# Kernel tuning notes

Hardware: AMD Instinct MI355X
Metric: run time of the kernel (lower is better)

The kernel has to match this reference:

```python
import jax, jax.numpy as jnp
import numpy as np

B = 1024      # batch
E = 1024      # encoding_dim
OUT = 34      # 17 joints x 2 coords


def setup_inputs() -> dict:
    key = jax.random.key(0)
    ks = jax.random.split(key, 8)
    s = 0.02  # weight init scale
    return {
        "h": jax.random.normal(ks[0], (B, E), dtype=jnp.float32),
        "c": jax.random.normal(ks[1], (B, E), dtype=jnp.float32),
        "W_ih": jax.random.normal(ks[2], (4 * E, E), dtype=jnp.float32) * s,
        "W_hh": jax.random.normal(ks[3], (4 * E, E), dtype=jnp.float32) * s,
        "b_ih": jax.random.normal(ks[4], (4 * E,), dtype=jnp.float32) * s,
        "b_hh": jax.random.normal(ks[5], (4 * E,), dtype=jnp.float32) * s,
        "W_out": jax.random.normal(ks[6], (OUT, E), dtype=jnp.float32) * s,
        "b_out": jax.random.normal(ks[7], (OUT,), dtype=jnp.float32) * s,
        "future_preds": 10,
    }


def reference(h, c, W_ih, W_hh, b_ih, b_hh, W_out, b_out, future_preds):
    E_ = h.shape[1]
    start = jnp.zeros_like(h)  # zeros=True start token

    def step(carry, _):
        h_t, c_t, x = carry
        # LSTMCell: gates in PyTorch order i, f, g, o
        gates = x @ W_ih.T + b_ih + h_t @ W_hh.T + b_hh  # [B, 4E]
        i = jax.nn.sigmoid(gates[:, 0 * E_:1 * E_])
        f = jax.nn.sigmoid(gates[:, 1 * E_:2 * E_])
        g = jnp.tanh(gates[:, 2 * E_:3 * E_])
        o = jax.nn.sigmoid(gates[:, 3 * E_:4 * E_])
        c_new = f * c_t + i * g
        h_new = o * jnp.tanh(c_new)
        return (h_new, c_new, h_new), h_new

    _, hs = jax.lax.scan(step, (h, c, start), None, length=future_preds)
    # hs: [T, B, E] -> [B, T, E]
    preds = jnp.transpose(hs, (1, 0, 2))
    return preds @ W_out.T + b_out  # [B, T, 34]
```

## Files before the change

kernel.cpp:

```cpp
#include <hip/hip_runtime.h>
#include <cstdint>
#include <cstddef>

#define E_DIM   1024
#define B_DIM   1024
#define HPITCH  1040
#define T_STEPS 10
#define OUT_DIM 34
#define OUT_PAD 48
#define HSTR    24
#define WSLICE  65536
#define HT_ROWS 256
#define DYN_LDS (WSLICE * 2 + HT_ROWS * HSTR * 2)
#define HSLOT  ((size_t)B_DIM * HPITCH)

typedef __attribute__((ext_vector_type(4))) float  f32x4;
typedef __attribute__((ext_vector_type(8))) __bf16 bf16x8;

__device__ __forceinline__ unsigned short f2bf(float f) {
    unsigned int u = __float_as_uint(f);
    u = (u + 0x7FFFu + ((u >> 16) & 1u)) >> 16;
    return (unsigned short)u;
}
__device__ __forceinline__ float sigmoid_(float x) { return 1.0f / (1.0f + __expf(-x)); }
__device__ __forceinline__ float tanh_(float x)    { return 2.0f / (1.0f + __expf(-2.0f * x)) - 1.0f; }

__global__ void prep_weights_frag(const float* __restrict__ W_ih, const float* __restrict__ W_hh,
                                  unsigned short* __restrict__ WsumF, unsigned short* __restrict__ WhhF) {
    const int bn = blockIdx.x >> 3, qtr = (blockIdx.x >> 1) & 3, half = blockIdx.x & 1;
    const int nt = threadIdx.x >> 6, lane = threadIdx.x & 63;
    const int j = lane & 15, q = lane >> 4;
    const int srow = nt * E_DIM + bn * 16 + j;
    const float* wi = W_ih + (size_t)srow * E_DIM;
    const float* wh = W_hh + (size_t)srow * E_DIM;
    const size_t dstb = (size_t)bn * 65536 + (size_t)qtr * 16384 + nt * 512 + lane * 8;
#pragma unroll
    for (int ks8i = 0; ks8i < 4; ++ks8i) {
        const int ks8 = half * 4 + ks8i;
        const int k = qtr * 256 + ks8 * 32 + q * 8;
        float4 i0 = *(const float4*)(wi + k);
        float4 i1 = *(const float4*)(wi + k + 4);
        float4 h0 = *(const float4*)(wh + k);
        float4 h1 = *(const float4*)(wh + k + 4);
        unsigned short* ds = WsumF + dstb + ks8 * 2048;
        unsigned short* dh = WhhF  + dstb + ks8 * 2048;
        ds[0] = f2bf(i0.x + h0.x); ds[1] = f2bf(i0.y + h0.y);
        ds[2] = f2bf(i0.z + h0.z); ds[3] = f2bf(i0.w + h0.w);
        ds[4] = f2bf(i1.x + h1.x); ds[5] = f2bf(i1.y + h1.y);
        ds[6] = f2bf(i1.z + h1.z); ds[7] = f2bf(i1.w + h1.w);
        dh[0] = f2bf(h0.x); dh[1] = f2bf(h0.y); dh[2] = f2bf(h0.z); dh[3] = f2bf(h0.w);
        dh[4] = f2bf(h1.x); dh[5] = f2bf(h1.y); dh[6] = f2bf(h1.z); dh[7] = f2bf(h1.w);
    }
}

__global__ void prep_state(const float* __restrict__ h0, const float* __restrict__ c0,
                           const float* __restrict__ W_out,
                           const float* __restrict__ b_ih, const float* __restrict__ b_hh,
                           unsigned short* __restrict__ hbuf, unsigned short* __restrict__ Woutp,
                           float* __restrict__ bperm, float* __restrict__ C) {
    const int b = blockIdx.x;
    const int t = threadIdx.x;
    if (b < 1024) {
        const size_t src = ((size_t)b * 256 + t) * 4;
        float4 hv = *(const float4*)(h0 + src);
        const size_t i = (size_t)b * HPITCH + t * 4;
        hbuf[i + 0] = f2bf(hv.x);
        hbuf[i + 1] = f2bf(hv.y);
        hbuf[i + 2] = f2bf(hv.z);
        hbuf[i + 3] = f2bf(hv.w);
    } else if (b < 1072) {
        const int o = b - 1024;
        const int k = t * 4;
        float4 w = make_float4(0.f, 0.f, 0.f, 0.f);
        if (o < OUT_DIM) w = *(const float4*)(W_out + (size_t)o * E_DIM + k);
        const size_t dst = (size_t)o * E_DIM + k;
        Woutp[dst + 0] = f2bf(w.x);
        Woutp[dst + 1] = f2bf(w.y);
        Woutp[dst + 2] = f2bf(w.z);
        Woutp[dst + 3] = f2bf(w.w);
    } else if (b < 1088) {
        const int n = (b - 1072) * 256 + t;
        const int g = (n >> 4) & 3;
        const int e = ((n >> 6) << 4) | (n & 15);
        const int srow = g * E_DIM + e;
        bperm[n] = b_ih[srow] + b_hh[srow];
    } else {
        const int m = b - 1088;
        const int e0 = t * 4;
        float4 v = *(const float4*)(c0 + (size_t)m * E_DIM + e0);
        const int bm = m >> 7, wave = (m >> 5) & 3, mt = (m >> 4) & 1, q = (m >> 2) & 3, r = m & 3;
        const float vv[4] = {v.x, v.y, v.z, v.w};
#pragma unroll
        for (int ii = 0; ii < 4; ++ii) {
            const int e = e0 + ii;
            const int bn = e >> 4, jj = e & 15;
            const int lane = q * 16 + jj;
            C[(((size_t)(bn * 8 + bm) * 4 + wave) * 64 + lane) * 8 + mt * 4 + r] = vv[ii];
        }
    }
}

__global__ __launch_bounds__(512, 2) void lstm_step(
    const unsigned short* __restrict__ WF,
    const float* __restrict__ bp,
    const unsigned short* __restrict__ Hin,
    float* __restrict__ C,
    unsigned short* __restrict__ Hout)
{
    extern __shared__ __align__(16) unsigned short smem[];
    unsigned short* Wlds = smem;
    unsigned short* Ht   = smem + WSLICE;

    const int tid  = threadIdx.x;
    const int w    = tid >> 6;
    const int lane = tid & 63;
    const int bn = blockIdx.x;
    const int g  = blockIdx.y;
    const int j  = lane & 15;
    const int q  = lane >> 4;

    f32x4 acc[2][4];
#pragma unroll
    for (int a = 0; a < 2; ++a)
#pragma unroll
        for (int b = 0; b < 4; ++b) acc[a][b] = (f32x4){0.f, 0.f, 0.f, 0.f};

    const int nb = bn * 64 + j;
    const float bi = bp[nb +  0];
    const float bf = bp[nb + 16];
    const float bg = bp[nb + 32];
    const float bo = bp[nb + 48];
    const int obm = g * 2 + (w >> 2), owv = w & 3;
    const size_t cbase = (((size_t)(bn * 8 + obm) * 4 + owv) * 64 + lane) * 8;
    float4 cold0 = *(const float4*)(C + cbase);
    float4 cold1 = *(const float4*)(C + cbase + 4);

    const unsigned short* arow0 = Hin + (size_t)(g * 256 + w * 32 + j) * HPITCH + q * 8;
    const unsigned short* arow1 = arow0 + (size_t)16 * HPITCH;
    const unsigned short* wsrc  = WF + (size_t)bn * WSLICE;

    {
        uint4 wreg[8];
#pragma unroll
        for (int r2 = 0; r2 < 2; ++r2) {
#pragma unroll
            for (int i = 0; i < 8; ++i)
                wreg[i] = *(const uint4*)(wsrc + ((r2 * 8 + i) * 512 + tid) * 8);
#pragma unroll
            for (int i = 0; i < 8; ++i)
                *(uint4*)(Wlds + ((r2 * 8 + i) * 512 + tid) * 8) = wreg[i];
        }
    }

    uint4 ra[8][2];
#pragma unroll
    for (int p = 0; p < 8; ++p) {
        ra[p][0] = *(const uint4*)(arow0 + p * 32);
        ra[p][1] = *(const uint4*)(arow1 + p * 32);
    }
    __syncthreads();

    for (int qtr = 0; qtr < 4; ++qtr) {
        const unsigned short* wb = Wlds + qtr * 16384 + lane * 8;
#pragma unroll
        for (int ks8 = 0; ks8 < 8; ++ks8) {
            const int ks = qtr * 8 + ks8;
            bf16x8 av0 = __builtin_bit_cast(bf16x8, ra[ks8][0]);
            bf16x8 av1 = __builtin_bit_cast(bf16x8, ra[ks8][1]);
            bf16x8 bv[4];
#pragma unroll
            for (int nt = 0; nt < 4; ++nt)
                bv[nt] = *(const bf16x8*)(wb + (ks8 * 4 + nt) * 512);
#pragma unroll
            for (int nt = 0; nt < 4; ++nt) {
                acc[0][nt] = __builtin_amdgcn_mfma_f32_16x16x32_bf16(av0, bv[nt], acc[0][nt], 0, 0, 0);
                acc[1][nt] = __builtin_amdgcn_mfma_f32_16x16x32_bf16(av1, bv[nt], acc[1][nt], 0, 0, 0);
            }
            if (ks < 24) {
                ra[ks8][0] = *(const uint4*)(arow0 + (ks + 8) * 32);
                ra[ks8][1] = *(const uint4*)(arow1 + (ks + 8) * 32);
            }
        }
    }

    float4 cnew[2];
    const float coldv[2][4] = {{cold0.x, cold0.y, cold0.z, cold0.w},
                               {cold1.x, cold1.y, cold1.z, cold1.w}};
#pragma unroll
    for (int mt = 0; mt < 2; ++mt) {
#pragma unroll
        for (int r = 0; r < 4; ++r) {
            const float iv = sigmoid_(acc[mt][0][r] + bi);
            const float fv = sigmoid_(acc[mt][1][r] + bf);
            const float gv = tanh_(acc[mt][2][r] + bg);
            const float ov = sigmoid_(acc[mt][3][r] + bo);
            const float cn = fv * coldv[mt][r] + iv * gv;
            cnew[mt][r] = cn;
            const int rowl = w * 32 + mt * 16 + q * 4 + r;
            Ht[rowl * HSTR + j] = f2bf(ov * tanh_(cn));
        }
    }
    *(float4*)(C + cbase)     = cnew[0];
    *(float4*)(C + cbase + 4) = cnew[1];
    __syncthreads();

    {
        const int row = tid >> 1, part = tid & 1;
        uint4 v = *(const uint4*)(Ht + row * HSTR + part * 8);
        *(uint4*)(Hout + (size_t)(g * 256 + row) * HPITCH + bn * 16 + part * 8) = v;
    }
}

__global__ __launch_bounds__(256) void proj_kernel(
    const unsigned short* __restrict__ Hs,
    const unsigned short* __restrict__ Wo,
    const float* __restrict__ b_out,
    float* __restrict__ Out)
{
    __shared__ float red[4][32][OUT_PAD];

    const int tid = threadIdx.x, wave = tid >> 6, lane = tid & 63;
    const int j = lane & 15, q = lane >> 4;
    const int t  = blockIdx.y;
    const int bb = blockIdx.x;
    const unsigned short* Hbase = Hs + (size_t)t * HSLOT + (size_t)bb * 32 * HPITCH;
    const int k0 = wave * 256;

    f32x4 acc[2][3];
#pragma unroll
    for (int a = 0; a < 2; ++a)
#pragma unroll
        for (int b = 0; b < 3; ++b) acc[a][b] = (f32x4){0.f, 0.f, 0.f, 0.f};

#pragma unroll
    for (int kk = 0; kk < 256; kk += 32) {
        const int kc = k0 + kk + q * 8;
        bf16x8 av[2], bv[3];
#pragma unroll
        for (int mt = 0; mt < 2; ++mt)
            av[mt] = *(const bf16x8*)(Hbase + (size_t)(mt * 16 + j) * HPITCH + kc);
#pragma unroll
        for (int nt = 0; nt < 3; ++nt)
            bv[nt] = *(const bf16x8*)(Wo + (size_t)(nt * 16 + j) * E_DIM + kc);
#pragma unroll
        for (int mt = 0; mt < 2; ++mt)
#pragma unroll
            for (int nt = 0; nt < 3; ++nt)
                acc[mt][nt] = __builtin_amdgcn_mfma_f32_16x16x32_bf16(av[mt], bv[nt], acc[mt][nt], 0, 0, 0);
    }

#pragma unroll
    for (int mt = 0; mt < 2; ++mt)
#pragma unroll
        for (int nt = 0; nt < 3; ++nt)
#pragma unroll
            for (int r = 0; r < 4; ++r)
                red[wave][mt * 16 + q * 4 + r][nt * 16 + j] = acc[mt][nt][r];
    __syncthreads();

#pragma unroll
    for (int ii = 0; ii < 6; ++ii) {
        const int idx = tid * 6 + ii;
        const int row = idx / OUT_PAD, o = idx % OUT_PAD;
        if (o < OUT_DIM) {
            const float s = red[0][row][o] + red[1][row][o] + red[2][row][o] + red[3][row][o];
            Out[((size_t)(bb * 32 + row) * T_STEPS + t) * OUT_DIM + o] = s + b_out[o];
        }
    }
}

extern "C" void kernel_launch(void* const* d_in, const int* in_sizes, int n_in,
                              void* d_out, int out_size, void* d_ws, size_t ws_size,
                              hipStream_t stream) {
    (void)in_sizes; (void)n_in; (void)out_size; (void)ws_size;
    const float* h     = (const float*)d_in[0];
    const float* c     = (const float*)d_in[1];
    const float* W_ih  = (const float*)d_in[2];
    const float* W_hh  = (const float*)d_in[3];
    const float* b_ih  = (const float*)d_in[4];
    const float* b_hh  = (const float*)d_in[5];
    const float* W_out = (const float*)d_in[6];
    const float* b_out = (const float*)d_in[7];
    float* out = (float*)d_out;

    char* ws = (char*)d_ws;
    unsigned short* WsumF = (unsigned short*)(ws + 0);
    unsigned short* WhhF  = (unsigned short*)(ws + 8388608);
    float*          bperm = (float*)(ws + 16777216);
    unsigned short* Woutp = (unsigned short*)(ws + 16842752);
    float*          cbuf  = (float*)(ws + 16941056);
    unsigned short* hs    = (unsigned short*)(ws + 21135360);

    hipFuncSetAttribute((const void*)lstm_step,
                        hipFuncAttributeMaxDynamicSharedMemorySize, DYN_LDS);

    prep_weights_frag<<<512, 256, 0, stream>>>(W_ih, W_hh, WsumF, WhhF);
    prep_state<<<2112, 256, 0, stream>>>(h, c, W_out, b_ih, b_hh, hs, Woutp, bperm, cbuf);

    lstm_step<<<dim3(64, 4), 512, DYN_LDS, stream>>>(WhhF, bperm, hs, cbuf, hs + HSLOT);
    for (int t = 1; t < T_STEPS; ++t)
        lstm_step<<<dim3(64, 4), 512, DYN_LDS, stream>>>(WsumF, bperm,
                                                         hs + (size_t)t * HSLOT,
                                                         cbuf,
                                                         hs + (size_t)(t + 1) * HSLOT);

    proj_kernel<<<dim3(32, T_STEPS), 256, 0, stream>>>(hs + HSLOT, Woutp, b_out, out);
}
```

Measured before the change: 275.6 us.

## Overlap second-half weight load with MFMA compute and merge prep kernels

The step kernel now stages only the first half of its weight slice into LDS before computing. The second half is fetched into registers while the first half's MFMAs run, then written to LDS after a barrier, hiding part of the global load latency. The two prep kernels are also merged into one launch to save launch overhead. The trade-off is an extra barrier mid-loop and longer register live ranges across the first half of the compute.

New measurement: 367.5 us. +33.4%, slower.

```diff
diff --git a/kernel.cpp b/kernel.cpp
--- a/kernel.cpp
+++ b/kernel.cpp
@@ -10,6 +10,7 @@
 #define OUT_PAD 48
 #define HSTR    24
 #define WSLICE  65536
+#define WHALF   32768
 #define HT_ROWS 256
 #define DYN_LDS (WSLICE * 2 + HT_ROWS * HSTR * 2)
 #define HSLOT  ((size_t)B_DIM * HPITCH)
@@ -25,41 +26,43 @@
 __device__ __forceinline__ float sigmoid_(float x) { return 1.0f / (1.0f + __expf(-x)); }
 __device__ __forceinline__ float tanh_(float x)    { return 2.0f / (1.0f + __expf(-2.0f * x)) - 1.0f; }
 
-__global__ void prep_weights_frag(const float* __restrict__ W_ih, const float* __restrict__ W_hh,
-                                  unsigned short* __restrict__ WsumF, unsigned short* __restrict__ WhhF) {
-    const int bn = blockIdx.x >> 3, qtr = (blockIdx.x >> 1) & 3, half = blockIdx.x & 1;
-    const int nt = threadIdx.x >> 6, lane = threadIdx.x & 63;
-    const int j = lane & 15, q = lane >> 4;
-    const int srow = nt * E_DIM + bn * 16 + j;
-    const float* wi = W_ih + (size_t)srow * E_DIM;
-    const float* wh = W_hh + (size_t)srow * E_DIM;
-    const size_t dstb = (size_t)bn * 65536 + (size_t)qtr * 16384 + nt * 512 + lane * 8;
-#pragma unroll
-    for (int ks8i = 0; ks8i < 4; ++ks8i) {
-        const int ks8 = half * 4 + ks8i;
-        const int k = qtr * 256 + ks8 * 32 + q * 8;
-        float4 i0 = *(const float4*)(wi + k);
-        float4 i1 = *(const float4*)(wi + k + 4);
-        float4 h0 = *(const float4*)(wh + k);
-        float4 h1 = *(const float4*)(wh + k + 4);
-        unsigned short* ds = WsumF + dstb + ks8 * 2048;
-        unsigned short* dh = WhhF  + dstb + ks8 * 2048;
-        ds[0] = f2bf(i0.x + h0.x); ds[1] = f2bf(i0.y + h0.y);
-        ds[2] = f2bf(i0.z + h0.z); ds[3] = f2bf(i0.w + h0.w);
-        ds[4] = f2bf(i1.x + h1.x); ds[5] = f2bf(i1.y + h1.y);
-        ds[6] = f2bf(i1.z + h1.z); ds[7] = f2bf(i1.w + h1.w);
-        dh[0] = f2bf(h0.x); dh[1] = f2bf(h0.y); dh[2] = f2bf(h0.z); dh[3] = f2bf(h0.w);
-        dh[4] = f2bf(h1.x); dh[5] = f2bf(h1.y); dh[6] = f2bf(h1.z); dh[7] = f2bf(h1.w);
-    }
-}
-
-__global__ void prep_state(const float* __restrict__ h0, const float* __restrict__ c0,
-                           const float* __restrict__ W_out,
-                           const float* __restrict__ b_ih, const float* __restrict__ b_hh,
-                           unsigned short* __restrict__ hbuf, unsigned short* __restrict__ Woutp,
-                           float* __restrict__ bperm, float* __restrict__ C) {
-    const int b = blockIdx.x;
+__global__ void prep_all(const float* __restrict__ W_ih, const float* __restrict__ W_hh,
+                         const float* __restrict__ h0, const float* __restrict__ c0,
+                         const float* __restrict__ W_out,
+                         const float* __restrict__ b_ih, const float* __restrict__ b_hh,
+                         unsigned short* __restrict__ WsumF, unsigned short* __restrict__ WhhF,
+                         unsigned short* __restrict__ hbuf, unsigned short* __restrict__ Woutp,
+                         float* __restrict__ bperm, float* __restrict__ C) {
+    const int blk = blockIdx.x;
     const int t = threadIdx.x;
+    if (blk < 512) {
+        const int bn = blk >> 3, qtr = (blk >> 1) & 3, half = blk & 1;
+        const int nt = t >> 6, lane = t & 63;
+        const int j = lane & 15, q = lane >> 4;
+        const int srow = nt * E_DIM + bn * 16 + j;
+        const float* wi = W_ih + (size_t)srow * E_DIM;
+        const float* wh = W_hh + (size_t)srow * E_DIM;
+        const size_t dstb = (size_t)bn * 65536 + (size_t)qtr * 16384 + nt * 512 + lane * 8;
+#pragma unroll
+        for (int ks8i = 0; ks8i < 4; ++ks8i) {
+            const int ks8 = half * 4 + ks8i;
+            const int k = qtr * 256 + ks8 * 32 + q * 8;
+            float4 i0 = *(const float4*)(wi + k);
+            float4 i1 = *(const float4*)(wi + k + 4);
+            float4 h0v = *(const float4*)(wh + k);
+            float4 h1v = *(const float4*)(wh + k + 4);
+            unsigned short* ds = WsumF + dstb + ks8 * 2048;
+            unsigned short* dh = WhhF  + dstb + ks8 * 2048;
+            ds[0] = f2bf(i0.x + h0v.x); ds[1] = f2bf(i0.y + h0v.y);
+            ds[2] = f2bf(i0.z + h0v.z); ds[3] = f2bf(i0.w + h0v.w);
+            ds[4] = f2bf(i1.x + h1v.x); ds[5] = f2bf(i1.y + h1v.y);
+            ds[6] = f2bf(i1.z + h1v.z); ds[7] = f2bf(i1.w + h1v.w);
+            dh[0] = f2bf(h0v.x); dh[1] = f2bf(h0v.y); dh[2] = f2bf(h0v.z); dh[3] = f2bf(h0v.w);
+            dh[4] = f2bf(h1v.x); dh[5] = f2bf(h1v.y); dh[6] = f2bf(h1v.z); dh[7] = f2bf(h1v.w);
+        }
+        return;
+    }
+    const int b = blk - 512;
     if (b < 1024) {
         const size_t src = ((size_t)b * 256 + t) * 4;
         float4 hv = *(const float4*)(h0 + src);
@@ -139,18 +142,13 @@
     const unsigned short* arow1 = arow0 + (size_t)16 * HPITCH;
     const unsigned short* wsrc  = WF + (size_t)bn * WSLICE;
 
-    {
-        uint4 wreg[8];
-#pragma unroll
-        for (int r2 = 0; r2 < 2; ++r2) {
-#pragma unroll
-            for (int i = 0; i < 8; ++i)
-                wreg[i] = *(const uint4*)(wsrc + ((r2 * 8 + i) * 512 + tid) * 8);
-#pragma unroll
-            for (int i = 0; i < 8; ++i)
-                *(uint4*)(Wlds + ((r2 * 8 + i) * 512 + tid) * 8) = wreg[i];
-        }
-    }
+    uint4 wreg[8];
+#pragma unroll
+    for (int i = 0; i < 8; ++i)
+        wreg[i] = *(const uint4*)(wsrc + (i * 512 + tid) * 8);
+#pragma unroll
+    for (int i = 0; i < 8; ++i)
+        *(uint4*)(Wlds + (i * 512 + tid) * 8) = wreg[i];
 
     uint4 ra[8][2];
 #pragma unroll
@@ -160,26 +158,41 @@
     }
     __syncthreads();
 
-    for (int qtr = 0; qtr < 4; ++qtr) {
-        const unsigned short* wb = Wlds + qtr * 16384 + lane * 8;
-#pragma unroll
-        for (int ks8 = 0; ks8 < 8; ++ks8) {
-            const int ks = qtr * 8 + ks8;
-            bf16x8 av0 = __builtin_bit_cast(bf16x8, ra[ks8][0]);
-            bf16x8 av1 = __builtin_bit_cast(bf16x8, ra[ks8][1]);
-            bf16x8 bv[4];
-#pragma unroll
-            for (int nt = 0; nt < 4; ++nt)
-                bv[nt] = *(const bf16x8*)(wb + (ks8 * 4 + nt) * 512);
-#pragma unroll
-            for (int nt = 0; nt < 4; ++nt) {
-                acc[0][nt] = __builtin_amdgcn_mfma_f32_16x16x32_bf16(av0, bv[nt], acc[0][nt], 0, 0, 0);
-                acc[1][nt] = __builtin_amdgcn_mfma_f32_16x16x32_bf16(av1, bv[nt], acc[1][nt], 0, 0, 0);
+    for (int half = 0; half < 2; ++half) {
+        if (half == 0) {
+#pragma unroll
+            for (int i = 0; i < 8; ++i)
+                wreg[i] = *(const uint4*)(wsrc + WHALF + (i * 512 + tid) * 8);
+        }
+#pragma unroll
+        for (int qq = 0; qq < 2; ++qq) {
+            const int qtr = half * 2 + qq;
+            const unsigned short* wb = Wlds + qtr * 16384 + lane * 8;
+#pragma unroll
+            for (int ks8 = 0; ks8 < 8; ++ks8) {
+                const int ks = qtr * 8 + ks8;
+                bf16x8 av0 = __builtin_bit_cast(bf16x8, ra[ks8][0]);
+                bf16x8 av1 = __builtin_bit_cast(bf16x8, ra[ks8][1]);
+                bf16x8 bv[4];
+#pragma unroll
+                for (int nt = 0; nt < 4; ++nt)
+                    bv[nt] = *(const bf16x8*)(wb + (ks8 * 4 + nt) * 512);
+#pragma unroll
+                for (int nt = 0; nt < 4; ++nt) {
+                    acc[0][nt] = __builtin_amdgcn_mfma_f32_16x16x32_bf16(av0, bv[nt], acc[0][nt], 0, 0, 0);
+                    acc[1][nt] = __builtin_amdgcn_mfma_f32_16x16x32_bf16(av1, bv[nt], acc[1][nt], 0, 0, 0);
+                }
+                if (ks < 24) {
+                    ra[ks8][0] = *(const uint4*)(arow0 + (ks + 8) * 32);
+                    ra[ks8][1] = *(const uint4*)(arow1 + (ks + 8) * 32);
+                }
             }
-            if (ks < 24) {
-                ra[ks8][0] = *(const uint4*)(arow0 + (ks + 8) * 32);
-                ra[ks8][1] = *(const uint4*)(arow1 + (ks + 8) * 32);
-            }
+        }
+        if (half == 0) {
+#pragma unroll
+            for (int i = 0; i < 8; ++i)
+                *(uint4*)(Wlds + WHALF + (i * 512 + tid) * 8) = wreg[i];
+            __syncthreads();
         }
     }
 
@@ -294,8 +307,8 @@
     hipFuncSetAttribute((const void*)lstm_step,
                         hipFuncAttributeMaxDynamicSharedMemorySize, DYN_LDS);
 
-    prep_weights_frag<<<512, 256, 0, stream>>>(W_ih, W_hh, WsumF, WhhF);
-    prep_state<<<2112, 256, 0, stream>>>(h, c, W_out, b_ih, b_hh, hs, Woutp, bperm, cbuf);
+    prep_all<<<2624, 256, 0, stream>>>(W_ih, W_hh, h, c, W_out, b_ih, b_hh,
+                                       WsumF, WhhF, hs, Woutp, bperm, cbuf);
 
     lstm_step<<<dim3(64, 4), 512, DYN_LDS, stream>>>(WhhF, bperm, hs, cbuf, hs + HSLOT);
     for (int t = 1; t < T_STEPS; ++t)
```
